# Kernel tuning notes

Hardware: AMD Instinct MI355X
Metric: run time of the kernel (lower is better)

Reference implementation:

```python
import jax, jax.numpy as jnp
import numpy as np

WINDOW = 5  # window_size from init
C_COARSE = 256
C_FINE = 128


def _gather_windows(fine_nchw, b, lin_idx, stride, pad, w, wc):
    """Extract [M, w*w, C] windows centered on coarse grid cells.

    Equivalent to F.unfold(kernel=w, stride=stride, padding=pad) followed by
    rearrange('n (c ww) l -> n l ww c') and fancy-indexing [b, lin_idx],
    but gathers only the matched windows.
    """
    x = jnp.pad(fine_nchw, ((0, 0), (0, 0), (pad, pad), (pad, pad)))
    x = jnp.transpose(x, (0, 2, 3, 1))  # [N, Hp, Wp, C]
    r = lin_idx // wc
    c = lin_idx % wc
    offs = jnp.arange(w)
    rows = r[:, None] * stride + offs  # [M, w] (start = r*stride - pad, +pad shift)
    cols = c[:, None] * stride + offs  # [M, w]
    patches = x[b[:, None, None], rows[:, :, None], cols[:, None, :]]  # [M, w, w, C]
    return patches.reshape(patches.shape[0], w * w, patches.shape[-1])


def setup_inputs() -> dict:
    key = jax.random.key(0)
    ks = jax.random.split(key, 10)
    N, Hc, Hf, M = 2, 60, 240, 3000
    inp = {
        "coarse_image_feature_1": jax.random.normal(ks[0], (N, Hc * Hc, C_COARSE), jnp.float32),
        "coarse_image_feature_2": jax.random.normal(ks[1], (N, Hc * Hc, C_COARSE), jnp.float32),
        "fine_image_feature_1": jax.random.normal(ks[2], (N, C_FINE, Hf, Hf), jnp.float32),
        "fine_image_feature_2": jax.random.normal(ks[3], (N, C_FINE, Hf, Hf), jnp.float32),
        "batch_indices": jax.random.randint(ks[4], (M,), 0, N),
        "row_indices": jax.random.randint(ks[5], (M,), 0, Hc * Hc),
        "column_indices": jax.random.randint(ks[6], (M,), 0, Hc * Hc),
        "fine_height_width": Hf,
        "coarse_height_width": Hc,
        # learned params (kaiming-normal-ish weights, zero biases)
        "W_dp": jax.random.normal(ks[7], (C_FINE, C_COARSE), jnp.float32) * np.sqrt(2.0 / C_FINE),
        "b_dp": jnp.zeros((C_FINE,), jnp.float32),
        "W_merge": jax.random.normal(ks[8], (C_FINE, 2 * C_FINE), jnp.float32) * np.sqrt(2.0 / C_FINE),
        "b_merge": jnp.zeros((C_FINE,), jnp.float32),
    }
    return inp


def reference(coarse_image_feature_1, coarse_image_feature_2,
              fine_image_feature_1, fine_image_feature_2,
              batch_indices, row_indices, column_indices,
              fine_height_width, coarse_height_width,
              W_dp, b_dp, W_merge, b_merge):
    stride = fine_height_width // coarse_height_width
    pad = WINDOW // 2
    M = batch_indices.shape[0]

    f1 = _gather_windows(fine_image_feature_1, batch_indices, row_indices,
                         stride, pad, WINDOW, coarse_height_width)       # [M, ww, Cf]
    f2 = _gather_windows(fine_image_feature_2, batch_indices, column_indices,
                         stride, pad, WINDOW, coarse_height_width)       # [M, ww, Cf]

    coarse = jnp.concatenate([
        coarse_image_feature_1[batch_indices, row_indices],
        coarse_image_feature_2[batch_indices, column_indices],
    ], axis=0)                                                           # [2M, Cc]
    coarse = coarse @ W_dp.T + b_dp                                      # [2M, Cf]

    fine = jnp.concatenate([f1, f2], axis=0)                             # [2M, ww, Cf]
    combined = jnp.concatenate(
        [fine, jnp.broadcast_to(coarse[:, None, :], fine.shape)], axis=-1)  # [2M, ww, 2Cf]
    merged = combined @ W_merge.T + b_merge                              # [2M, ww, Cf]
    return merged[:M], merged[M:]
```

## Files before the change

### kernel.cpp

```cpp
#include <hip/hip_runtime.h>

#define HF 240
#define HC 60
#define STRIDEF 4
#define PADW 2
#define WIN 5
#define CC 256
#define CF 128
#define NPOS 25
#define NPX (HF*HF)
#define MPB 16
#define TPX 128
#define KCH 32
#define NCHK 4

typedef __bf16 bf16x8 __attribute__((ext_vector_type(8)));
typedef __bf16 bf16x4 __attribute__((ext_vector_type(4)));
typedef float  f32x4  __attribute__((ext_vector_type(4)));
typedef float  f32x2  __attribute__((ext_vector_type(2)));

__global__ void k_prep(const float* __restrict__ W_dp, const float* __restrict__ b_dp,
                       const float* __restrict__ W_merge, const float* __restrict__ b_merge,
                       __bf16* __restrict__ Wm1h, float* __restrict__ W_effT,
                       float* __restrict__ b_eff) {
    const int j = blockIdx.x;
    const int k = threadIdx.x;
    const float* wm2 = W_merge + (size_t)j * (2 * CF) + CF;

    float acc = 0.f, accb = 0.f;
    for (int q = 0; q < CF; ++q) {
        const float wq = wm2[q];
        acc  += wq * W_dp[(size_t)q * CC + k];
        accb += wq * b_dp[q];
    }
    W_effT[(size_t)k * CF + j] = acc;

    if (k < CF)
        Wm1h[(size_t)j * CF + k] = (__bf16)W_merge[(size_t)j * (2 * CF) + k];
    if (k == 0)
        b_eff[j] = accb + b_merge[j];
}

__global__ void k_coarse(const float* __restrict__ c1, const float* __restrict__ c2,
                         const int* __restrict__ bidx, const int* __restrict__ ridx,
                         const int* __restrict__ cidx, int M,
                         const float* __restrict__ W_effT, const float* __restrict__ b_eff,
                         float* __restrict__ c_all) {
    const int m0 = blockIdx.x * MPB;
    const int j  = threadIdx.x;
    const int twoM = 2 * M;
    __shared__ float v[MPB * CC];

    const int nm = (twoM - m0) < MPB ? (twoM - m0) : MPB;
    for (int mm = 0; mm < nm; ++mm) {
        int m = m0 + mm;
        const float* src;
        if (m < M) src = c1 + ((size_t)bidx[m] * (HC * HC) + ridx[m]) * CC;
        else       src = c2 + ((size_t)bidx[m - M] * (HC * HC) + cidx[m - M]) * CC;
        v[mm * CC + j]      = src[j];
        v[mm * CC + j + CF] = src[j + CF];
    }
    __syncthreads();

    float acc[MPB];
    const float be = b_eff[j];
    #pragma unroll
    for (int mm = 0; mm < MPB; ++mm) acc[mm] = be;

    for (int k = 0; k < CC; k += 4) {
        float w0 = W_effT[(k + 0) * CF + j];
        float w1 = W_effT[(k + 1) * CF + j];
        float w2 = W_effT[(k + 2) * CF + j];
        float w3 = W_effT[(k + 3) * CF + j];
        #pragma unroll
        for (int mm = 0; mm < MPB; ++mm) {
            const f32x4 vv = *(const f32x4*)&v[mm * CC + k];
            acc[mm] += w0 * vv.x + w1 * vv.y + w2 * vv.z + w3 * vv.w;
        }
    }
    for (int mm = 0; mm < nm; ++mm)
        c_all[(size_t)(m0 + mm) * CF + j] = acc[mm];
}

__global__ __launch_bounds__(256) void k_tgemm(
    const float* __restrict__ f1, const float* __restrict__ f2,
    const __bf16* __restrict__ Wm1h, __bf16* __restrict__ V) {

    const int slot = blockIdx.y;
    const float* src = (slot >= 2 ? f2 : f1) + (size_t)(slot & 1) * CF * NPX;
    const int px0 = blockIdx.x * TPX;
    const int t  = threadIdx.x;
    const int l  = t & 63;
    const int w  = t >> 6;
    const int lo16 = l & 15;
    const int hi   = l >> 4;

    __shared__ __attribute__((aligned(16))) __bf16 chk[2][(TPX / 2) * 64];

    bf16x8 bfrag[2][NCHK];
    #pragma unroll
    for (int nt2 = 0; nt2 < 2; ++nt2) {
        const int j = w * 32 + 2 * lo16 + nt2;
        #pragma unroll
        for (int c = 0; c < NCHK; ++c)
            bfrag[nt2][c] = *reinterpret_cast<const bf16x8*>(
                Wm1h + (size_t)j * CF + c * KCH + hi * 8);
    }

    f32x2 vva[8], vvb[8];

#define LOAD_CHUNK(c, vbuf)                                                    \
    {                                                                          \
        const int ch0 = (c) * KCH + w * 8;                                     \
        _Pragma("unroll")                                                      \
        for (int e = 0; e < 8; ++e)                                            \
            vbuf[e] = *reinterpret_cast<const f32x2*>(                         \
                src + (size_t)(ch0 + e) * NPX + px0 + 2 * l);                  \
    }

#define WRITE_CHUNK(buf, vbuf)                                                 \
    {                                                                          \
        _Pragma("unroll")                                                      \
        for (int i = 0; i < 2; ++i) {                                          \
            const int px = 2 * l + i;                                          \
            bf16x8 pk;                                                         \
            _Pragma("unroll")                                                  \
            for (int e = 0; e < 8; ++e) pk[e] = (__bf16)vbuf[e][i];            \
            const int rp = px >> 1;                                  \
            const int S  = (w * 2 + (px & 1)) ^ (rp & 7);                      \
            *reinterpret_cast<bf16x8*>(&chk[buf][rp * 64 + S * 8]) = pk;       \
        }                                                                      \
    }

    f32x4 acc[8][2];
    #pragma unroll
    for (int mt = 0; mt < 8; ++mt) {
        acc[mt][0] = (f32x4){0.f, 0.f, 0.f, 0.f};
        acc[mt][1] = (f32x4){0.f, 0.f, 0.f, 0.f};
    }

    LOAD_CHUNK(0, vva);

    #pragma unroll
    for (int c = 0; c < NCHK; ++c) {
        const int buf = c & 1;
        if (buf == 0) {
            if (c + 1 < NCHK) LOAD_CHUNK(c + 1, vvb);
            WRITE_CHUNK(0, vva);
        } else {
            if (c + 1 < NCHK) LOAD_CHUNK(c + 1, vva);
            WRITE_CHUNK(1, vvb);
        }
        __syncthreads();

        #pragma unroll
        for (int mt = 0; mt < 8; ++mt) {
            const int px = mt * 16 + lo16;
            const int rp = px >> 1;
            const int S  = (hi * 2 + (px & 1)) ^ (rp & 7);
            const bf16x8 a = *reinterpret_cast<const bf16x8*>(&chk[buf][rp * 64 + S * 8]);
            acc[mt][0] = __builtin_amdgcn_mfma_f32_16x16x32_bf16(a, bfrag[0][c], acc[mt][0], 0, 0, 0);
            acc[mt][1] = __builtin_amdgcn_mfma_f32_16x16x32_bf16(a, bfrag[1][c], acc[mt][1], 0, 0, 0);
        }
        __syncthreads();
    }

    uint* Vp = (uint*)(V + ((size_t)slot * NPX + px0) * CF);
    const int dcol = w * 16 + lo16;
    #pragma unroll
    for (int mt = 0; mt < 8; ++mt) {
        #pragma unroll
        for (int reg = 0; reg < 4; ++reg) {
            const int px = mt * 16 + hi * 4 + reg;
            union { uint u; __bf16 h[2]; } cv;
            cv.h[0] = (__bf16)acc[mt][0][reg];
            cv.h[1] = (__bf16)acc[mt][1][reg];
            Vp[(size_t)px * 64 + dcol] = cv.u;
        }
    }
#undef LOAD_CHUNK
#undef WRITE_CHUNK
}

__global__ __launch_bounds__(256) void k_gather(
    const __bf16* __restrict__ V,
    const int* __restrict__ bidx, const int* __restrict__ ridx,
    const int* __restrict__ cidx, int M,
    const float* __restrict__ c_all, float* __restrict__ out) {

    const int m = blockIdx.x;
    const int t = threadIdx.x;
    const int g  = t >> 5;
    const int l32 = t & 31;

    int b, lin, ii;
    if (m < M) { ii = 0; b = bidx[m];     lin = ridx[m]; }
    else       { ii = 1; b = bidx[m - M]; lin = cidx[m - M]; }
    const int slot = ii * 2 + b;
    const int r  = lin / HC, c = lin - r * HC;
    const int y0 = r * STRIDEF - PADW;
    const int x0 = c * STRIDEF - PADW;

    const f32x4 c4 = *reinterpret_cast<const f32x4*>(c_all + (size_t)m * CF + l32 * 4);
    const __bf16* Vb = V + (size_t)slot * NPX * CF;
    float* ob = out + (size_t)m * (NPOS * CF) + l32 * 4;

    #pragma unroll
    for (int pass = 0; pass < 4; ++pass) {
        const int p = pass * 8 + g;
        if (p < NPOS) {
            const int wy = (p * 13) >> 6;
            const int wx = p - wy * WIN;
            const int y = y0 + wy, x = x0 + wx;
            f32x4 o = c4;
            if (y >= 0 && x >= 0) {
                const bf16x4 v = *reinterpret_cast<const bf16x4*>(Vb + (size_t)(y * HF + x) * CF + l32 * 4);
                o.x += (float)v.x; o.y += (float)v.y; o.z += (float)v.z; o.w += (float)v.w;
            }
            *reinterpret_cast<f32x4*>(ob + (size_t)p * CF) = o;
        }
    }
}

__global__ __launch_bounds__(256) void k_main_direct(
    const float* __restrict__ f1, const float* __restrict__ f2,
    const int* __restrict__ bidx, const int* __restrict__ ridx,
    const int* __restrict__ cidx, int M,
    const __bf16* __restrict__ Wm1h, const float* __restrict__ c_all,
    float* __restrict__ out) {

    const int m = blockIdx.x;
    const int t = threadIdx.x;
    const int l    = t & 63;
    const int wv   = t >> 6;
    const int lo16 = l & 15;
    const int hi   = l >> 4;

    __shared__ __bf16 patch[32 * CF];

    bf16x8 bfrag[2][4];
    #pragma unroll
    for (int nt2 = 0; nt2 < 2; ++nt2) {
        const int j = wv * 32 + nt2 * 16 + lo16;
        #pragma unroll
        for (int kt = 0; kt < 4; ++kt)
            bfrag[nt2][kt] = *reinterpret_cast<const bf16x8*>(Wm1h + (size_t)j * CF + kt * 32 + hi * 8);
    }

    const float* img; int b, lin;
    if (m < M) { img = f1; b = bidx[m];     lin = ridx[m]; }
    else       { img = f2; b = bidx[m - M]; lin = cidx[m - M]; }
    const int r  = lin / HC, c = lin - r * HC;
    const int y0 = r * STRIDEF - PADW;
    const int x0 = c * STRIDEF - PADW;

    for (int task = t; task < CF * WIN; task += 256) {
        const int ch = task / WIN;
        const int wy = task - ch * WIN;
        const int y  = y0 + wy;
        const bool yok = (y >= 0);
        const float* rowp = img + (((size_t)b * CF + ch) * HF + (yok ? y : 0)) * HF;
        #pragma unroll
        for (int wx = 0; wx < WIN; ++wx) {
            const int x = x0 + wx;
            const float val = (yok && x >= 0) ? rowp[x] : 0.f;
            const int pos = wy * WIN + wx;
            patch[pos * CF + (ch ^ ((pos & 7) << 3))] = (__bf16)val;
        }
    }
    __syncthreads();

    f32x4 acc[2][2];
    #pragma unroll
    for (int mt = 0; mt < 2; ++mt)
        #pragma unroll
        for (int nt2 = 0; nt2 < 2; ++nt2)
            acc[mt][nt2] = (f32x4){0.f, 0.f, 0.f, 0.f};

    const int swz = (lo16 & 7) << 3;
    #pragma unroll
    for (int kt = 0; kt < 4; ++kt) {
        const int koff = (kt * 32 + hi * 8) ^ swz;
        bf16x8 a0 = *reinterpret_cast<const bf16x8*>(&patch[ lo16       * CF + koff]);
        bf16x8 a1 = *reinterpret_cast<const bf16x8*>(&patch[(16 + lo16) * CF + koff]);
        #pragma unroll
        for (int nt2 = 0; nt2 < 2; ++nt2) {
            acc[0][nt2] = __builtin_amdgcn_mfma_f32_16x16x32_bf16(a0, bfrag[nt2][kt], acc[0][nt2], 0, 0, 0);
            acc[1][nt2] = __builtin_amdgcn_mfma_f32_16x16x32_bf16(a1, bfrag[nt2][kt], acc[1][nt2], 0, 0, 0);
        }
    }

    float* ob = out + (size_t)m * (NPOS * CF);
    #pragma unroll
    for (int nt2 = 0; nt2 < 2; ++nt2) {
        const int j  = wv * 32 + nt2 * 16 + lo16;
        const float cv = c_all[(size_t)m * CF + j];
        #pragma unroll
        for (int mt = 0; mt < 2; ++mt) {
            #pragma unroll
            for (int reg = 0; reg < 4; ++reg) {
                const int p = mt * 16 + hi * 4 + reg;
                if (p < NPOS)
                    ob[(size_t)p * CF + j] = acc[mt][nt2][reg] + cv;
            }
        }
    }
}

extern "C" void kernel_launch(void* const* d_in, const int* in_sizes, int n_in,
                              void* d_out, int out_size, void* d_ws, size_t ws_size,
                              hipStream_t stream) {
    const float* c1      = (const float*)d_in[0];
    const float* c2      = (const float*)d_in[1];
    const float* f1      = (const float*)d_in[2];
    const float* f2      = (const float*)d_in[3];
    const int*   bidx    = (const int*)d_in[4];
    const int*   ridx    = (const int*)d_in[5];
    const int*   cidx    = (const int*)d_in[6];
    const float* W_dp    = (const float*)d_in[9];
    const float* b_dp    = (const float*)d_in[10];
    const float* W_merge = (const float*)d_in[11];
    const float* b_merge = (const float*)d_in[12];
    const int M = in_sizes[4];

    char* ws = (char*)d_ws;
    __bf16* Wm1h  = (__bf16*)(ws);
    float* W_effT = (float*)(ws + (64 << 10));
    float* b_eff  = (float*)(ws + (192 << 10));
    float* c_all  = (float*)(ws + (256 << 10));
    __bf16* V     = (__bf16*)(ws + (4 << 20));

    const size_t need_V = (size_t)(4 << 20) + (size_t)4 * NPX * CF * 2;

    hipLaunchKernelGGL(k_prep, dim3(CF), dim3(CC), 0, stream,
                       W_dp, b_dp, W_merge, b_merge, Wm1h, W_effT, b_eff);
    hipLaunchKernelGGL(k_coarse, dim3((2 * M + MPB - 1) / MPB), dim3(CF), 0, stream,
                       c1, c2, bidx, ridx, cidx, M, W_effT, b_eff, c_all);

    if (ws_size >= need_V) {
        hipLaunchKernelGGL(k_tgemm, dim3(NPX / TPX, 4), dim3(256), 0, stream,
                           f1, f2, Wm1h, V);
        hipLaunchKernelGGL(k_gather, dim3(2 * M), dim3(256), 0, stream,
                           V, bidx, ridx, cidx, M, c_all, (float*)d_out);
    } else {
        hipLaunchKernelGGL(k_main_direct, dim3(2 * M), dim3(256), 0, stream,
                           f1, f2, bidx, ridx, cidx, M, Wm1h, c_all, (float*)d_out);
    }
}
```

Baseline: 95.34 us.

## Stage fine-feature chunks via direct global-to-LDS loads in fp32

The transform GEMM kernel now copies fp32 feature chunks straight into shared memory with global_load_lds and an XOR swizzle. Conversion to bf16 moves to the LDS read side, replacing the earlier register-staged load, convert and pack path. Weight fragments are loaded per chunk instead of all up front, and launch bounds request 4 blocks per CU to lower register pressure and raise occupancy. In exchange, LDS use doubles because fp32 is stored, and each MFMA operand now takes 8 scalar LDS reads plus conversions instead of one vector read.

```diff
diff --git a/kernel.cpp b/kernel.cpp
--- a/kernel.cpp
+++ b/kernel.cpp
@@ -11,13 +11,10 @@
 #define NPX (HF*HF)
 #define MPB 16
 #define TPX 128
-#define KCH 32
-#define NCHK 4
 
 typedef __bf16 bf16x8 __attribute__((ext_vector_type(8)));
 typedef __bf16 bf16x4 __attribute__((ext_vector_type(4)));
 typedef float  f32x4  __attribute__((ext_vector_type(4)));
-typedef float  f32x2  __attribute__((ext_vector_type(2)));
 
 __global__ void k_prep(const float* __restrict__ W_dp, const float* __restrict__ b_dp,
                        const float* __restrict__ W_merge, const float* __restrict__ b_merge,
@@ -82,7 +79,7 @@
         c_all[(size_t)(m0 + mm) * CF + j] = acc[mm];
 }
 
-__global__ __launch_bounds__(256) void k_tgemm(
+__global__ __launch_bounds__(256, 4) void k_tgemm(
     const float* __restrict__ f1, const float* __restrict__ f2,
     const __bf16* __restrict__ Wm1h, __bf16* __restrict__ V) {
 
@@ -95,41 +92,25 @@
     const int lo16 = l & 15;
     const int hi   = l >> 4;
 
-    __shared__ __attribute__((aligned(16))) __bf16 chk[2][(TPX / 2) * 64];
-
-    bf16x8 bfrag[2][NCHK];
-    #pragma unroll
-    for (int nt2 = 0; nt2 < 2; ++nt2) {
-        const int j = w * 32 + 2 * lo16 + nt2;
-        #pragma unroll
-        for (int c = 0; c < NCHK; ++c)
-            bfrag[nt2][c] = *reinterpret_cast<const bf16x8*>(
-                Wm1h + (size_t)j * CF + c * KCH + hi * 8);
-    }
-
-    f32x2 vva[8], vvb[8];
-
-#define LOAD_CHUNK(c, vbuf)                                                    \
-    {                                                                          \
-        const int ch0 = (c) * KCH + w * 8;                                     \
-        _Pragma("unroll")                                                      \
-        for (int e = 0; e < 8; ++e)                                            \
-            vbuf[e] = *reinterpret_cast<const f32x2*>(                         \
-                src + (size_t)(ch0 + e) * NPX + px0 + 2 * l);                  \
-    }
-
-#define WRITE_CHUNK(buf, vbuf)                                                 \
-    {                                                                          \
-        _Pragma("unroll")                                                      \
-        for (int i = 0; i < 2; ++i) {                                          \
-            const int px = 2 * l + i;                                          \
-            bf16x8 pk;                                                         \
-            _Pragma("unroll")                                                  \
-            for (int e = 0; e < 8; ++e) pk[e] = (__bf16)vbuf[e][i];            \
-            const int rp = px >> 1;                                  \
-            const int S  = (w * 2 + (px & 1)) ^ (rp & 7);                      \
-            *reinterpret_cast<bf16x8*>(&chk[buf][rp * 64 + S * 8]) = pk;       \
-        }                                                                      \
+    __shared__ __attribute__((aligned(16))) float chkf[2][32 * TPX];
+
+    const int seg = l >> 5;
+    const int q4  = (l & 31) * 4;
+
+#define STAGE(c, b)                                                           \
+    {                                                                         \
+        _Pragma("unroll")                                                     \
+        for (int ii = 0; ii < 4; ++ii) {                                      \
+            const int i   = w * 4 + ii;                                       \
+            const int chl = 2 * i + seg;                                      \
+            const int ch  = (c) * 32 + chl;                                   \
+            const int pxg = q4 ^ (((ch >> 3) & 3) << 4);                      \
+            const float* gp = src + (size_t)ch * NPX + px0 + pxg;             \
+            __builtin_amdgcn_global_load_lds(                                 \
+                (const __attribute__((address_space(1))) void*)gp,            \
+                (__attribute__((address_space(3))) void*)&chkf[b][i * 256],   \
+                16, 0, 0);                                                    \
+        }                                                                     \
     }
 
     f32x4 acc[8][2];
@@ -139,31 +120,32 @@
         acc[mt][1] = (f32x4){0.f, 0.f, 0.f, 0.f};
     }
 
-    LOAD_CHUNK(0, vva);
-
-    #pragma unroll
-    for (int c = 0; c < NCHK; ++c) {
-        const int buf = c & 1;
-        if (buf == 0) {
-            if (c + 1 < NCHK) LOAD_CHUNK(c + 1, vvb);
-            WRITE_CHUNK(0, vva);
-        } else {
-            if (c + 1 < NCHK) LOAD_CHUNK(c + 1, vva);
-            WRITE_CHUNK(1, vvb);
-        }
+    STAGE(0, 0);
+
+    #pragma unroll
+    for (int c = 0; c < 4; ++c) {
+        const int b = c & 1;
+        if (c < 3) STAGE(c + 1, b ^ 1);
         __syncthreads();
 
+        const bf16x8 bf0 = *reinterpret_cast<const bf16x8*>(
+            Wm1h + (size_t)(w * 32 + 2 * lo16 + 0) * CF + c * 32 + hi * 8);
+        const bf16x8 bf1 = *reinterpret_cast<const bf16x8*>(
+            Wm1h + (size_t)(w * 32 + 2 * lo16 + 1) * CF + c * 32 + hi * 8);
+
         #pragma unroll
         for (int mt = 0; mt < 8; ++mt) {
-            const int px = mt * 16 + lo16;
-            const int rp = px >> 1;
-            const int S  = (hi * 2 + (px & 1)) ^ (rp & 7);
-            const bf16x8 a = *reinterpret_cast<const bf16x8*>(&chk[buf][rp * 64 + S * 8]);
-            acc[mt][0] = __builtin_amdgcn_mfma_f32_16x16x32_bf16(a, bfrag[0][c], acc[mt][0], 0, 0, 0);
-            acc[mt][1] = __builtin_amdgcn_mfma_f32_16x16x32_bf16(a, bfrag[1][c], acc[mt][1], 0, 0, 0);
+            const int pxr = (mt * 16 + lo16) ^ (hi << 4);
+            bf16x8 a;
+            #pragma unroll
+            for (int e = 0; e < 8; ++e)
+                a[e] = (__bf16)chkf[b][(hi * 8 + e) * TPX + pxr];
+            acc[mt][0] = __builtin_amdgcn_mfma_f32_16x16x32_bf16(a, bf0, acc[mt][0], 0, 0, 0);
+            acc[mt][1] = __builtin_amdgcn_mfma_f32_16x16x32_bf16(a, bf1, acc[mt][1], 0, 0, 0);
         }
         __syncthreads();
     }
+#undef STAGE
 
     uint* Vp = (uint*)(V + ((size_t)slot * NPX + px0) * CF);
     const int dcol = w * 16 + lo16;
@@ -178,8 +160,6 @@
             Vp[(size_t)px * 64 + dcol] = cv.u;
         }
     }
-#undef LOAD_CHUNK
-#undef WRITE_CHUNK
 }
 
 __global__ __launch_bounds__(256) void k_gather(
```

After: 95.31 us. Within noise of the previous version (-0.0%).
